# Performance work log

Measured on AMD Instinct MI355X. Metric: run time of the kernel, lower is better.

Reference implementation:

```python
import jax, jax.numpy as jnp
import numpy as np

NPOINT, RADIUS, NSAMPLE = 1024, 0.2, 32
BN_EPS = 1e-5


def _fps(xyz, npoint):
    """Farthest point sampling. xyz: [B,N,3] -> idx [B,npoint]. Deterministic seed (point 0)."""
    B, N, _ = xyz.shape
    init = (jnp.full((B, N), 1e10, xyz.dtype), jnp.zeros((B,), jnp.int32))

    def step(carry, _):
        distance, farthest = carry
        centroid = jnp.take_along_axis(xyz, farthest[:, None, None], axis=1)  # [B,1,3]
        dist = jnp.sum((xyz - centroid) ** 2, -1)                              # [B,N]
        distance = jnp.minimum(distance, dist)
        nxt = jnp.argmax(distance, axis=-1).astype(jnp.int32)
        return (distance, nxt), farthest

    _, cents = jax.lax.scan(step, init, None, length=npoint)  # [npoint,B]
    return cents.T  # [B,npoint]


def _gather(points, idx):
    """points [B,N,C], idx [B,...] -> [B,...,C] (batched fancy indexing)."""
    return jax.vmap(lambda p, i: p[i])(points, idx)


def _square_distance(src, dst):
    # [B,S,3] x [B,N,3] -> [B,S,N]
    d = -2.0 * jnp.einsum('bsc,bnc->bsn', src, dst)
    d += jnp.sum(src ** 2, -1)[:, :, None]
    d += jnp.sum(dst ** 2, -1)[:, None, :]
    return d


def _query_ball(radius, nsample, xyz, new_xyz):
    B, N, _ = xyz.shape
    sqr = _square_distance(new_xyz, xyz)                      # [B,S,N]
    base = jnp.arange(N, dtype=jnp.int32)[None, None, :]
    idx = jnp.where(sqr > radius ** 2, N, base)
    idx = jnp.sort(idx, axis=-1)[:, :, :nsample]              # [B,S,K]
    first = idx[:, :, 0:1]
    idx = jnp.where(idx == N, first, idx)
    return jnp.clip(idx, 0, N - 1)


def _mlp_bn_relu(h, w, b, g, be):
    # h: [B,S,K,Cin]; 1x1 conv == matmul; BN (training-mode batch stats) over (B,S,K).
    y = jnp.einsum('bskc,cd->bskd', h, w) + b
    mu = jnp.mean(y, axis=(0, 1, 2))
    var = jnp.var(y, axis=(0, 1, 2))
    y = (y - mu) * jax.lax.rsqrt(var + BN_EPS) * g + be
    return jax.nn.relu(y)


def setup_inputs():
    key = jax.random.key(0)
    ks = jax.random.split(key, 8)
    B, N, D = 16, 4096, 64
    xyz = jax.random.uniform(ks[0], (B, 3, N), jnp.float32)           # points in unit cube
    points = jax.random.normal(ks[1], (B, D, N), jnp.float32)
    c = [3 + D, 64, 64, 128]
    w0 = jax.random.normal(ks[2], (c[0], c[1]), jnp.float32) * 0.1
    w1 = jax.random.normal(ks[3], (c[1], c[2]), jnp.float32) * 0.1
    w2 = jax.random.normal(ks[4], (c[2], c[3]), jnp.float32) * 0.1
    b0 = jax.random.normal(ks[5], (c[1],), jnp.float32) * 0.05
    b1 = jax.random.normal(ks[6], (c[2],), jnp.float32) * 0.05
    b2 = jax.random.normal(ks[7], (c[3],), jnp.float32) * 0.05
    return dict(xyz=xyz, points=points,
                w0=w0, b0=b0, g0=jnp.ones(c[1]), be0=jnp.zeros(c[1]),
                w1=w1, b1=b1, g1=jnp.ones(c[2]), be1=jnp.zeros(c[2]),
                w2=w2, b2=b2, g2=jnp.ones(c[3]), be2=jnp.zeros(c[3]))


def reference(xyz, points, w0, b0, g0, be0, w1, b1, g1, be1, w2, b2, g2, be2):
    xyz_t = jnp.transpose(xyz, (0, 2, 1))       # [B,N,3]
    pts_t = jnp.transpose(points, (0, 2, 1))    # [B,N,D]
    B, N, _ = xyz_t.shape

    fps_idx = _fps(xyz_t, NPOINT)                               # [B,S]
    new_xyz = _gather(xyz_t, fps_idx)                           # [B,S,3]
    idx = _query_ball(RADIUS, NSAMPLE, xyz_t, new_xyz)          # [B,S,K]
    grouped_xyz = _gather(xyz_t, idx) - new_xyz[:, :, None, :]  # [B,S,K,3]
    grouped_pts = _gather(pts_t, idx)                           # [B,S,K,D]
    h = jnp.concatenate([grouped_xyz, grouped_pts], axis=-1)    # [B,S,K,3+D]

    h = _mlp_bn_relu(h, w0, b0, g0, be0)
    h = _mlp_bn_relu(h, w1, b1, g1, be1)
    h = _mlp_bn_relu(h, w2, b2, g2, be2)
    new_points = jnp.max(h, axis=2)                             # [B,S,Cout]

    return jnp.transpose(new_xyz, (0, 2, 1)), jnp.transpose(new_points, (0, 2, 1))
```

## Files before the change

### kernel.cpp

```cpp
#include <hip/hip_runtime.h>
#include <hip/hip_bf16.h>

typedef unsigned short u16;
typedef short short8 __attribute__((ext_vector_type(8)));
typedef float f32x4 __attribute__((ext_vector_type(4)));

#define NBLK_PASS 4096

#define WS_XYZT   0u
#define WS_PTSH   786432u
#define WS_PTSL   (WS_PTSH + 8388608u)
#define WS_NEWXYZ (WS_PTSL + 8388608u)
#define WS_BALL   (WS_NEWXYZ + 196608u)
#define WS_W0F    (WS_BALL + 2097152u)
#define WS_W1F    (WS_W0F + 24576u)
#define WS_W2F    (WS_W1F + 16384u)
#define WS_P0     (WS_W2F + 32768u)
#define WS_P1     (WS_P0 + 2097152u)
#define WS_P2     (WS_P1 + 2097152u)
#define WS_PR     (WS_P2 + 4194304u)
#define WS_AC0    (WS_PR + 65536u)
#define WS_AC1    (WS_AC0 + 1024u)
#define WS_AC2    (WS_AC1 + 1024u)

__device__ __forceinline__ void split2(float v, u16& h, u16& l) {
  __hip_bfloat16 bh = __float2bfloat16(v);
  float r = v - __bfloat162float(bh);
  __hip_bfloat16 bl = __float2bfloat16(r);
  h = *reinterpret_cast<u16*>(&bh);
  l = *reinterpret_cast<u16*>(&bl);
}

__global__ __launch_bounds__(256) void front_k(
    const float* __restrict__ xyz, const float* __restrict__ pts,
    const float* __restrict__ w0, const float* __restrict__ w1, const float* __restrict__ w2,
    float* __restrict__ xyzT, u16* __restrict__ ptsH, u16* __restrict__ ptsL,
    float* __restrict__ newxyz, float* __restrict__ out0,
    u16* __restrict__ w0f, u16* __restrict__ w1f, u16* __restrict__ w2f)
{
  __shared__ __align__(16) char sm[53312];
  int bid = blockIdx.x, tid = threadIdx.x;

  if (bid < 16) {
    float* lx = (float*)sm; float* ly = lx + 4096; float* lz = ly + 4096;
    int* sIdx = (int*)(sm + 49152);
    unsigned long long* red = (unsigned long long*)(sm + 53248);
    int b = bid, lane = tid & 63, wid = tid >> 6;
    const float4* sx = (const float4*)(xyz + (size_t)(b*3 + 0)*4096);
    const float4* sy = (const float4*)(xyz + (size_t)(b*3 + 1)*4096);
    const float4* sz = (const float4*)(xyz + (size_t)(b*3 + 2)*4096);
    for (int i = tid; i < 1024; i += 256) {
      ((float4*)lx)[i] = sx[i]; ((float4*)ly)[i] = sy[i]; ((float4*)lz)[i] = sz[i];
    }
    __syncthreads();
    float px[16], py[16], pz[16], dist[16];
    #pragma unroll
    for (int i = 0; i < 16; ++i) {
      int p = tid + 256*i;
      px[i] = lx[p]; py[i] = ly[p]; pz[i] = lz[p]; dist[i] = 1e10f;
    }
    unsigned int lo0 = 4095u - (unsigned int)tid;
    int far = 0;
    for (int t = 0; t < 1024; ++t) {
      if (tid == 0) sIdx[t] = far;
      if (t == 1023) break;
      float cx = lx[far], cy = ly[far], cz = lz[far];
      unsigned long long bk = 0ull;
      #pragma unroll
      for (int i = 0; i < 16; ++i) {
        float dx = __fsub_rn(px[i], cx);
        float dy = __fsub_rn(py[i], cy);
        float dz = __fsub_rn(pz[i], cz);
        float d = __fadd_rn(__fadd_rn(__fmul_rn(dx,dx), __fmul_rn(dy,dy)), __fmul_rn(dz,dz));
        float nd = fminf(dist[i], d);
        dist[i] = nd;
        unsigned long long k = ((unsigned long long)__float_as_uint(nd) << 32) | (unsigned long long)(lo0 - 256u*i);
        if (k > bk) bk = k;
      }
      for (int off = 1; off < 64; off <<= 1) {
        unsigned long long o = __shfl_xor(bk, off, 64);
        if (o > bk) bk = o;
      }
      if (lane == 0) red[(t & 1)*4 + wid] = bk;
      __syncthreads();
      unsigned long long m = red[(t & 1)*4 + 0];
      #pragma unroll
      for (int w = 1; w < 4; ++w) { unsigned long long o = red[(t & 1)*4 + w]; if (o > m) m = o; }
      far = 4095 - (int)(unsigned int)(m & 0xffffffffull);
    }
    __syncthreads();
    for (int t = tid; t < 1024; t += 256) {
      int fi = sIdx[t];
      float x = lx[fi], y = ly[fi], z = lz[fi];
      size_t nb = ((size_t)b*1024 + t)*3;
      newxyz[nb + 0] = x; newxyz[nb + 1] = y; newxyz[nb + 2] = z;
      out0[(size_t)(b*3 + 0)*1024 + t] = x;
      out0[(size_t)(b*3 + 1)*1024 + t] = y;
      out0[(size_t)(b*3 + 2)*1024 + t] = z;
    }
  } else if (bid == 16) {
    for (int e = tid; e < 6144; e += 256) {
      int j = e & 7, l = (e >> 3) & 63, ct = (e >> 9) & 3, ks = e >> 11;
      int kk = ks*32 + (l >> 4)*8 + j, col = ct*16 + (l & 15);
      float v = 0.f;
      if (kk < 67) { int orow = (kk < 64) ? (kk + 3) : (kk - 64); v = w0[orow*64 + col]; }
      u16 h, lo; split2(v, h, lo);
      w0f[e] = h; w0f[6144 + e] = lo;
    }
    for (int e = tid; e < 4096; e += 256) {
      int j = e & 7, l = (e >> 3) & 63, ct = (e >> 9) & 3, ks = e >> 11;
      int kk = ks*32 + (l >> 4)*8 + j, col = ct*16 + (l & 15);
      u16 h, lo; split2(w1[kk*64 + col], h, lo);
      w1f[e] = h; w1f[4096 + e] = lo;
    }
    for (int e = tid; e < 8192; e += 256) {
      int j = e & 7, l = (e >> 3) & 63, ct = (e >> 9) & 3, ks = (e >> 11) & 1, cg = e >> 12;
      int kk = ks*32 + (l >> 4)*8 + j, col = cg*64 + ct*16 + (l & 15);
      u16 h, lo; split2(w2[kk*128 + col], h, lo);
      w2f[e] = h; w2f[8192 + e] = lo;
    }
  } else if (bid < 273) {
    int i = (bid - 17)*256 + tid;
    int b = i >> 12, n = i & 4095;
    float x = xyz[(b*3 + 0)*4096 + n];
    float y = xyz[(b*3 + 1)*4096 + n];
    float z = xyz[(b*3 + 2)*4096 + n];
    xyzT[(size_t)i*3 + 0] = x; xyzT[(size_t)i*3 + 1] = y; xyzT[(size_t)i*3 + 2] = z;
  } else {
    int bx = bid - 273;
    u16* th = (u16*)sm;
    u16* tl = th + 64*68;
    int b = bx >> 6, nt = bx & 63;
    int j = tid & 63, dq = tid >> 6;
    #pragma unroll
    for (int db = 0; db < 16; ++db) {
      int d = db*4 + dq;
      float v = pts[((size_t)(b*64 + d))*4096 + nt*64 + j];
      u16 h, lo; split2(v, h, lo);
      th[j*68 + d] = h; tl[j*68 + d] = lo;
    }
    __syncthreads();
    int row = tid >> 2, q = tid & 3;
    size_t o = ((size_t)(b*4096 + nt*64 + row))*64 + q*16;
    const u16* sh = th + row*68 + q*16;
    const u16* sl = tl + row*68 + q*16;
    #pragma unroll
    for (int i = 0; i < 4; ++i) {
      *(uint2*)(ptsH + o + i*4) = *(const uint2*)(sh + i*4);
      *(uint2*)(ptsL + o + i*4) = *(const uint2*)(sl + i*4);
    }
  }
}

__global__ __launch_bounds__(256) void ball_k(const float* __restrict__ xyz,
                                              const float* __restrict__ newxyz,
                                              int* __restrict__ ballidx) {
  __shared__ __align__(16) float lx[4096], ly[4096], lz[4096], ldn[4096];
  int b = blockIdx.x >> 5, tid = threadIdx.x, lane = tid & 63, wid = tid >> 6;
  const float4* sx = (const float4*)(xyz + (size_t)(b*3 + 0)*4096);
  const float4* sy = (const float4*)(xyz + (size_t)(b*3 + 1)*4096);
  const float4* sz = (const float4*)(xyz + (size_t)(b*3 + 2)*4096);
  for (int i = tid; i < 1024; i += 256) {
    ((float4*)lx)[i] = sx[i]; ((float4*)ly)[i] = sy[i]; ((float4*)lz)[i] = sz[i];
  }
  __syncthreads();
  for (int i = tid; i < 4096; i += 256) {
    float x = lx[i], y = ly[i], z = lz[i];
    ldn[i] = __fadd_rn(__fadd_rn(__fmul_rn(x,x), __fmul_rn(y,y)), __fmul_rn(z,z));
  }
  __syncthreads();
  int s0 = (blockIdx.x & 31)*32 + wid*8;
  for (int ci = 0; ci < 8; ++ci) {
    int s = s0 + ci;
    const float* cp = newxyz + ((size_t)b*1024 + s)*3;
    float cx = cp[0], cy = cp[1], cz = cp[2];
    float sn = __fadd_rn(__fadd_rn(__fmul_rn(cx,cx), __fmul_rn(cy,cy)), __fmul_rn(cz,cz));
    int* orow = ballidx + (((size_t)b << 10) + s)*32;
    int cnt = 0, first = -1;
    for (int ch = 0; ch < 64; ++ch) {
      int p = ch*64 + lane;
      float x = lx[p], y = ly[p], z = lz[p];
      float dot = __fmaf_rn(cz, z, __fmaf_rn(cy, y, __fmul_rn(cx, x)));
      float sqr = __fadd_rn(__fadd_rn(__fmul_rn(-2.0f, dot), sn), ldn[p]);
      bool in = !(sqr > 0.04f);
      unsigned long long mask = __ballot(in);
      if (first < 0 && mask) first = ch*64 + (__ffsll((long long)mask) - 1);
      int rank = cnt + __popcll(mask & ((1ull << lane) - 1ull));
      if (in && rank < 32) orow[rank] = p;
      cnt += __popcll(mask);
      if (cnt >= 32) break;
    }
    if (cnt < 32) {
      int fv = (first < 0) ? 4095 : first;
      if (lane >= cnt && lane < 32) orow[lane] = fv;
    }
  }
}

#define LOFF 6144

__device__ __forceinline__ void stats_fin(float* sSt, float* __restrict__ partial,
                                          int C, int tid, int bid) {
  __syncthreads();
  for (int c = tid; c < C; c += 256) {
    float s = sSt[c*2] + sSt[(128 + c)*2] + sSt[(256 + c)*2] + sSt[(384 + c)*2];
    float q = sSt[c*2 + 1] + sSt[(128 + c)*2 + 1] + sSt[(256 + c)*2 + 1] + sSt[(384 + c)*2 + 1];
    partial[(size_t)bid*2*C + c] = s;
    partial[(size_t)bid*2*C + C + c] = q;
  }
}

template<int DEPTH>
__global__ __launch_bounds__(256, 2) void pass_k(
    const int* __restrict__ ballidx,
    const u16* __restrict__ ptsH, const u16* __restrict__ ptsL,
    const float* __restrict__ xyzT, const float* __restrict__ newxyz,
    const u16* __restrict__ w0f, const u16* __restrict__ w1f, const u16* __restrict__ w2f,
    const float* __restrict__ b0, const float* __restrict__ b1, const float* __restrict__ b2,
    const float* __restrict__ ac0, const float* __restrict__ ac1, const float* __restrict__ ac2,
    float* __restrict__ partial, float* __restrict__ outPts)
{
  __shared__ __align__(16) u16 sAh[128*104];
  __shared__ __align__(16) u16 sAl[128*104];
  __shared__ __align__(16) u16 sW[12288];
  int tid = threadIdx.x, lane = tid & 63, wid = tid >> 6;
  int lrow = lane & 15, lkg = lane >> 4;
  int r0 = wid*32;

  {
    int r = tid >> 1, half = tid & 1;
    int R = blockIdx.x*128 + r;
    int b = R >> 15, s = (R & 32767) >> 5;
    int n = ballidx[R];
    size_t o = ((((size_t)b << 12) + n) << 6) + half*32;
    const uint4* srcH = (const uint4*)(ptsH + o);
    const uint4* srcL = (const uint4*)(ptsL + o);
    uint4* dH = (uint4*)(&sAh[r*104 + half*32]);
    uint4* dL = (uint4*)(&sAl[r*104 + half*32]);
    #pragma unroll
    for (int i = 0; i < 4; ++i) { dH[i] = srcH[i]; dL[i] = srcL[i]; }
    if (half) {
      uint4 zz; zz.x = zz.y = zz.z = zz.w = 0u;
      uint4* zH = (uint4*)(&sAh[r*104 + 64]);
      uint4* zL = (uint4*)(&sAl[r*104 + 64]);
      #pragma unroll
      for (int i = 0; i < 4; ++i) { zH[i] = zz; zL[i] = zz; }
      const float* xp = xyzT + (((size_t)b << 12) + n)*3;
      const float* cp = newxyz + (((size_t)b << 10) + s)*3;
      #pragma unroll
      for (int d = 0; d < 3; ++d) {
        u16 h, l; split2(__fsub_rn(xp[d], cp[d]), h, l);
        sAh[r*104 + 64 + d] = h; sAl[r*104 + 64 + d] = l;
      }
    }
  }
  for (int i = tid; i < 768; i += 256) {
    ((uint4*)sW)[i] = ((const uint4*)w0f)[i];
    *(uint4*)(sW + LOFF + i*8) = ((const uint4*)(w0f + 6144))[i];
  }
  __syncthreads();

  f32x4 zv = {0.f, 0.f, 0.f, 0.f};

  f32x4 acc[2][4];
  #pragma unroll
  for (int rt = 0; rt < 2; ++rt)
    #pragma unroll
    for (int ct = 0; ct < 4; ++ct) acc[rt][ct] = zv;
  #pragma unroll
  for (int ks = 0; ks < 3; ++ks) {
    short8 ah[2], al[2];
    #pragma unroll
    for (int rt = 0; rt < 2; ++rt) {
      int ro = (r0 + rt*16 + lrow)*104 + ks*32 + lkg*8;
      ah[rt] = *(const short8*)&sAh[ro];
      al[rt] = *(const short8*)&sAl[ro];
    }
    #pragma unroll
    for (int ct = 0; ct < 4; ++ct) {
      short8 wh = *(const short8*)&sW[((ks*4 + ct)*64 + lane)*8];
      short8 wl = *(const short8*)&sW[LOFF + ((ks*4 + ct)*64 + lane)*8];
      #pragma unroll
      for (int rt = 0; rt < 2; ++rt) {
        acc[rt][ct] = __builtin_amdgcn_mfma_f32_16x16x32_bf16(ah[rt], wh, acc[rt][ct], 0, 0, 0);
        acc[rt][ct] = __builtin_amdgcn_mfma_f32_16x16x32_bf16(al[rt], wh, acc[rt][ct], 0, 0, 0);
        acc[rt][ct] = __builtin_amdgcn_mfma_f32_16x16x32_bf16(ah[rt], wl, acc[rt][ct], 0, 0, 0);
      }
    }
  }

  if constexpr (DEPTH == 1) {
    __syncthreads();
    float* sSt = (float*)sW;
    #pragma unroll
    for (int ct = 0; ct < 4; ++ct) {
      int col = ct*16 + lrow;
      float bv = b0[col], s = 0.f, q = 0.f;
      #pragma unroll
      for (int rt = 0; rt < 2; ++rt)
        #pragma unroll
        for (int r = 0; r < 4; ++r) { float v = acc[rt][ct][r] + bv; s += v; q += v*v; }
      s += __shfl_xor(s, 16, 64); q += __shfl_xor(q, 16, 64);
      s += __shfl_xor(s, 32, 64); q += __shfl_xor(q, 32, 64);
      if (lane < 16) { sSt[(wid*128 + col)*2] = s; sSt[(wid*128 + col)*2 + 1] = q; }
    }
    stats_fin(sSt, partial, 64, tid, blockIdx.x);
    return;
  } else {
    __syncthreads();
    #pragma unroll
    for (int ct = 0; ct < 4; ++ct) {
      int col = ct*16 + lrow;
      float a = ac0[col], cc = fmaf(a, b0[col], ac0[64 + col]);
      #pragma unroll
      for (int rt = 0; rt < 2; ++rt)
        #pragma unroll
        for (int r = 0; r < 4; ++r) {
          float v = fmaxf(fmaf(a, acc[rt][ct][r], cc), 0.f);
          int row = r0 + rt*16 + lkg*4 + r;
          u16 h, l; split2(v, h, l);
          sAh[row*72 + col] = h; sAl[row*72 + col] = l;
        }
    }
    for (int i = tid; i < 512; i += 256) {
      ((uint4*)sW)[i] = ((const uint4*)w1f)[i];
      *(uint4*)(sW + LOFF + i*8) = ((const uint4*)(w1f + 4096))[i];
    }
    __syncthreads();

    #pragma unroll
    for (int rt = 0; rt < 2; ++rt)
      #pragma unroll
      for (int ct = 0; ct < 4; ++ct) acc[rt][ct] = zv;
    #pragma unroll
    for (int ks = 0; ks < 2; ++ks) {
      short8 ah[2], al[2];
      #pragma unroll
      for (int rt = 0; rt < 2; ++rt) {
        int ro = (r0 + rt*16 + lrow)*72 + ks*32 + lkg*8;
        ah[rt] = *(const short8*)&sAh[ro];
        al[rt] = *(const short8*)&sAl[ro];
      }
      #pragma unroll
      for (int ct = 0; ct < 4; ++ct) {
        short8 wh = *(const short8*)&sW[((ks*4 + ct)*64 + lane)*8];
        short8 wl = *(const short8*)&sW[LOFF + ((ks*4 + ct)*64 + lane)*8];
        #pragma unroll
        for (int rt = 0; rt < 2; ++rt) {
          acc[rt][ct] = __builtin_amdgcn_mfma_f32_16x16x32_bf16(ah[rt], wh, acc[rt][ct], 0, 0, 0);
          acc[rt][ct] = __builtin_amdgcn_mfma_f32_16x16x32_bf16(al[rt], wh, acc[rt][ct], 0, 0, 0);
          acc[rt][ct] = __builtin_amdgcn_mfma_f32_16x16x32_bf16(ah[rt], wl, acc[rt][ct], 0, 0, 0);
        }
      }
    }

    if constexpr (DEPTH == 2) {
      __syncthreads();
      float* sSt = (float*)sW;
      #pragma unroll
      for (int ct = 0; ct < 4; ++ct) {
        int col = ct*16 + lrow;
        float bv = b1[col], s = 0.f, q = 0.f;
        #pragma unroll
        for (int rt = 0; rt < 2; ++rt)
          #pragma unroll
          for (int r = 0; r < 4; ++r) { float v = acc[rt][ct][r] + bv; s += v; q += v*v; }
        s += __shfl_xor(s, 16, 64); q += __shfl_xor(q, 16, 64);
        s += __shfl_xor(s, 32, 64); q += __shfl_xor(q, 32, 64);
        if (lane < 16) { sSt[(wid*128 + col)*2] = s; sSt[(wid*128 + col)*2 + 1] = q; }
      }
      stats_fin(sSt, partial, 64, tid, blockIdx.x);
      return;
    } else {
      __syncthreads();
      #pragma unroll
      for (int ct = 0; ct < 4; ++ct) {
        int col = ct*16 + lrow;
        float a = ac1[col], cc = fmaf(a, b1[col], ac1[64 + col]);
        #pragma unroll
        for (int rt = 0; rt < 2; ++rt)
          #pragma unroll
          for (int r = 0; r < 4; ++r) {
            float v = fmaxf(fmaf(a, acc[rt][ct][r], cc), 0.f);
            int row = r0 + rt*16 + lkg*4 + r;
            u16 h, l; split2(v, h, l);
            sAh[row*72 + col] = h; sAl[row*72 + col] = l;
          }
      }
      for (int i = tid; i < 512; i += 256) {
        ((uint4*)sW)[i] = ((const uint4*)w2f)[i];
        *(uint4*)(sW + LOFF + i*8) = ((const uint4*)(w2f + 8192))[i];
      }
      __syncthreads();

      float sc[2][4], sq[2][4];
      #pragma unroll
      for (int cg = 0; cg < 2; ++cg) {
        if (cg) {
          __syncthreads();
          for (int i = tid; i < 512; i += 256) {
            ((uint4*)sW)[i] = ((const uint4*)(w2f + 4096))[i];
            *(uint4*)(sW + LOFF + i*8) = ((const uint4*)(w2f + 12288))[i];
          }
          __syncthreads();
        }
        f32x4 acc2[2][4];
        #pragma unroll
        for (int rt = 0; rt < 2; ++rt)
          #pragma unroll
          for (int ct = 0; ct < 4; ++ct) acc2[rt][ct] = zv;
        #pragma unroll
        for (int ks = 0; ks < 2; ++ks) {
          short8 ah[2], al[2];
          #pragma unroll
          for (int rt = 0; rt < 2; ++rt) {
            int ro = (r0 + rt*16 + lrow)*72 + ks*32 + lkg*8;
            ah[rt] = *(const short8*)&sAh[ro];
            al[rt] = *(const short8*)&sAl[ro];
          }
          #pragma unroll
          for (int ct = 0; ct < 4; ++ct) {
            short8 wh = *(const short8*)&sW[((ks*4 + ct)*64 + lane)*8];
            short8 wl = *(const short8*)&sW[LOFF + ((ks*4 + ct)*64 + lane)*8];
            #pragma unroll
            for (int rt = 0; rt < 2; ++rt) {
              acc2[rt][ct] = __builtin_amdgcn_mfma_f32_16x16x32_bf16(ah[rt], wh, acc2[rt][ct], 0, 0, 0);
              acc2[rt][ct] = __builtin_amdgcn_mfma_f32_16x16x32_bf16(al[rt], wh, acc2[rt][ct], 0, 0, 0);
              acc2[rt][ct] = __builtin_amdgcn_mfma_f32_16x16x32_bf16(ah[rt], wl, acc2[rt][ct], 0, 0, 0);
            }
          }
        }
        if constexpr (DEPTH == 3) {
          #pragma unroll
          for (int ct = 0; ct < 4; ++ct) {
            int col = cg*64 + ct*16 + lrow;
            float bv = b2[col], s = 0.f, q = 0.f;
            #pragma unroll
            for (int rt = 0; rt < 2; ++rt)
              #pragma unroll
              for (int r = 0; r < 4; ++r) { float v = acc2[rt][ct][r] + bv; s += v; q += v*v; }
            s += __shfl_xor(s, 16, 64); q += __shfl_xor(q, 16, 64);
            s += __shfl_xor(s, 32, 64); q += __shfl_xor(q, 32, 64);
            sc[cg][ct] = s; sq[cg][ct] = q;
          }
        } else {
          int G = blockIdx.x*4 + wid;
          int bb = G >> 10, ss = G & 1023;
          #pragma unroll
          for (int ct = 0; ct < 4; ++ct) {
            int col = cg*64 + ct*16 + lrow;
            float a = ac2[col], cc = fmaf(a, b2[col], ac2[128 + col]);
            float m = 0.f;
            #pragma unroll
            for (int rt = 0; rt < 2; ++rt)
              #pragma unroll
              for (int r = 0; r < 4; ++r)
                m = fmaxf(m, fmaxf(fmaf(a, acc2[rt][ct][r], cc), 0.f));
            m = fmaxf(m, __shfl_xor(m, 16, 64));
            m = fmaxf(m, __shfl_xor(m, 32, 64));
            if (lane < 16) outPts[((size_t)bb*128 + col)*1024 + ss] = m;
          }
        }
      }
      if constexpr (DEPTH == 3) {
        __syncthreads();
        float* sSt = (float*)sW;
        if (lane < 16) {
          #pragma unroll
          for (int cg = 0; cg < 2; ++cg)
            #pragma unroll
            for (int ct = 0; ct < 4; ++ct) {
              int col = cg*64 + ct*16 + lrow;
              sSt[(wid*128 + col)*2] = sc[cg][ct];
              sSt[(wid*128 + col)*2 + 1] = sq[cg][ct];
            }
        }
        stats_fin(sSt, partial, 128, tid, blockIdx.x);
      }
    }
  }
}

__global__ void r1_k(const float* __restrict__ partial, int C, float* __restrict__ pr) {
  int j = blockIdx.x, c = threadIdx.x;
  if (c < 2*C) {
    float s = 0.f;
    for (int i = 0; i < 64; ++i) s += partial[((size_t)(j*64 + i))*2*C + c];
    pr[j*2*C + c] = s;
  }
}
__global__ void r2_k(const float* __restrict__ pr, int C,
                     const float* __restrict__ g, const float* __restrict__ be,
                     float* __restrict__ ac) {
  int c = threadIdx.x;
  if (c < C) {
    float s = 0.f, q = 0.f;
    for (int j = 0; j < 64; ++j) { s += pr[j*2*C + c]; q += pr[j*2*C + C + c]; }
    const float inv = 1.0f / 524288.0f;
    float mu = s*inv, var = q*inv - mu*mu;
    float a = g[c] / sqrtf(var + 1e-5f);
    ac[c] = a; ac[C + c] = be[c] - mu*a;
  }
}

extern "C" void kernel_launch(void* const* d_in, const int* in_sizes, int n_in,
                              void* d_out, int out_size, void* d_ws, size_t ws_size,
                              hipStream_t stream) {
  const float* xyz = (const float*)d_in[0];
  const float* pts = (const float*)d_in[1];
  const float* w0  = (const float*)d_in[2];
  const float* b0  = (const float*)d_in[3];
  const float* g0  = (const float*)d_in[4];
  const float* be0 = (const float*)d_in[5];
  const float* w1  = (const float*)d_in[6];
  const float* b1  = (const float*)d_in[7];
  const float* g1  = (const float*)d_in[8];
  const float* be1 = (const float*)d_in[9];
  const float* w2  = (const float*)d_in[10];
  const float* b2  = (const float*)d_in[11];
  const float* g2  = (const float*)d_in[12];
  const float* be2 = (const float*)d_in[13];
  float* out = (float*)d_out;
  char* ws = (char*)d_ws;

  float* xyzT   = (float*)(ws + WS_XYZT);
  u16*   ptsH   = (u16*)(ws + WS_PTSH);
  u16*   ptsL   = (u16*)(ws + WS_PTSL);
  float* newxyz = (float*)(ws + WS_NEWXYZ);
  int*   ballix = (int*)(ws + WS_BALL);
  u16*   w0f    = (u16*)(ws + WS_W0F);
  u16*   w1f    = (u16*)(ws + WS_W1F);
  u16*   w2f    = (u16*)(ws + WS_W2F);
  float* p0     = (float*)(ws + WS_P0);
  float* p1     = (float*)(ws + WS_P1);
  float* p2     = (float*)(ws + WS_P2);
  float* pr     = (float*)(ws + WS_PR);
  float* ac0    = (float*)(ws + WS_AC0);
  float* ac1    = (float*)(ws + WS_AC1);
  float* ac2    = (float*)(ws + WS_AC2);
  float* outPts = out + 49152;

  front_k<<<1297, 256, 0, stream>>>(xyz, pts, w0, w1, w2, xyzT, ptsH, ptsL,
                                    newxyz, out, w0f, w1f, w2f);
  ball_k<<<512, 256, 0, stream>>>(xyz, newxyz, ballix);

  pass_k<1><<<NBLK_PASS, 256, 0, stream>>>(ballix, ptsH, ptsL, xyzT, newxyz,
      w0f, w1f, w2f, b0, b1, b2, ac0, ac1, ac2, p0, outPts);
  r1_k<<<64, 256, 0, stream>>>(p0, 64, pr);
  r2_k<<<1, 256, 0, stream>>>(pr, 64, g0, be0, ac0);

  pass_k<2><<<NBLK_PASS, 256, 0, stream>>>(ballix, ptsH, ptsL, xyzT, newxyz,
      w0f, w1f, w2f, b0, b1, b2, ac0, ac1, ac2, p1, outPts);
  r1_k<<<64, 256, 0, stream>>>(p1, 64, pr);
  r2_k<<<1, 256, 0, stream>>>(pr, 64, g1, be1, ac1);

  pass_k<3><<<NBLK_PASS, 256, 0, stream>>>(ballix, ptsH, ptsL, xyzT, newxyz,
      w0f, w1f, w2f, b0, b1, b2, ac0, ac1, ac2, p2, outPts);
  r1_k<<<64, 256, 0, stream>>>(p2, 128, pr);
  r2_k<<<1, 256, 0, stream>>>(pr, 128, g2, be2, ac2);

  pass_k<4><<<NBLK_PASS, 256, 0, stream>>>(ballix, ptsH, ptsL, xyzT, newxyz,
      w0f, w1f, w2f, b0, b1, b2, ac0, ac1, ac2, p2, outPts);
}
```

Before: 1.115 ms.

## Widen FPS block to 512 threads and use DPP wave reduction for argmax

The farthest-point-sampling front kernel now runs with 512 threads per block, so each thread holds 8 points instead of 16, which shortens the serial per-iteration work. The per-thread argmax now tracks a float and an index rather than packed 64-bit keys. The cross-lane reduction uses DPP row shifts and row broadcasts instead of xor shuffles, and the result is read from lane 63. The block-level reduction grows to 8 wave partials, and the other branches (weight packing, transpose, point split) are retuned for the larger block size. The trade-offs are more per-iteration barrier participants and possible changes in tie-breaking order.

```diff
diff --git a/kernel.cpp b/kernel.cpp
--- a/kernel.cpp
+++ b/kernel.cpp
@@ -31,14 +31,21 @@
   l = *reinterpret_cast<u16*>(&bl);
 }
 
-__global__ __launch_bounds__(256) void front_k(
+#define DPP_MAX64(CTRL) { \
+  unsigned int lo_ = (unsigned int)k, hi_ = (unsigned int)(k >> 32); \
+  unsigned int mlo_ = (unsigned int)__builtin_amdgcn_update_dpp(0, (int)lo_, CTRL, 0xF, 0xF, true); \
+  unsigned int mhi_ = (unsigned int)__builtin_amdgcn_update_dpp(0, (int)hi_, CTRL, 0xF, 0xF, true); \
+  unsigned long long m_ = ((unsigned long long)mhi_ << 32) | mlo_; \
+  if (m_ > k) k = m_; }
+
+__global__ __launch_bounds__(512) void front_k(
     const float* __restrict__ xyz, const float* __restrict__ pts,
     const float* __restrict__ w0, const float* __restrict__ w1, const float* __restrict__ w2,
     float* __restrict__ xyzT, u16* __restrict__ ptsH, u16* __restrict__ ptsL,
     float* __restrict__ newxyz, float* __restrict__ out0,
     u16* __restrict__ w0f, u16* __restrict__ w1f, u16* __restrict__ w2f)
 {
-  __shared__ __align__(16) char sm[53312];
+  __shared__ __align__(16) char sm[53376];
   int bid = blockIdx.x, tid = threadIdx.x;
 
   if (bid < 16) {
@@ -49,14 +56,14 @@
     const float4* sx = (const float4*)(xyz + (size_t)(b*3 + 0)*4096);
     const float4* sy = (const float4*)(xyz + (size_t)(b*3 + 1)*4096);
     const float4* sz = (const float4*)(xyz + (size_t)(b*3 + 2)*4096);
-    for (int i = tid; i < 1024; i += 256) {
+    for (int i = tid; i < 1024; i += 512) {
       ((float4*)lx)[i] = sx[i]; ((float4*)ly)[i] = sy[i]; ((float4*)lz)[i] = sz[i];
     }
     __syncthreads();
-    float px[16], py[16], pz[16], dist[16];
-    #pragma unroll
-    for (int i = 0; i < 16; ++i) {
-      int p = tid + 256*i;
+    float px[8], py[8], pz[8], dist[8];
+    #pragma unroll
+    for (int i = 0; i < 8; ++i) {
+      int p = tid + 512*i;
       px[i] = lx[p]; py[i] = ly[p]; pz[i] = lz[p]; dist[i] = 1e10f;
     }
     unsigned int lo0 = 4095u - (unsigned int)tid;
@@ -65,31 +72,30 @@
       if (tid == 0) sIdx[t] = far;
       if (t == 1023) break;
       float cx = lx[far], cy = ly[far], cz = lz[far];
-      unsigned long long bk = 0ull;
-      #pragma unroll
-      for (int i = 0; i < 16; ++i) {
+      float bestnd = -1.f; unsigned int bestlow = 0u;
+      #pragma unroll
+      for (int i = 0; i < 8; ++i) {
         float dx = __fsub_rn(px[i], cx);
         float dy = __fsub_rn(py[i], cy);
         float dz = __fsub_rn(pz[i], cz);
         float d = __fadd_rn(__fadd_rn(__fmul_rn(dx,dx), __fmul_rn(dy,dy)), __fmul_rn(dz,dz));
         float nd = fminf(dist[i], d);
         dist[i] = nd;
-        unsigned long long k = ((unsigned long long)__float_as_uint(nd) << 32) | (unsigned long long)(lo0 - 256u*i);
-        if (k > bk) bk = k;
-      }
-      for (int off = 1; off < 64; off <<= 1) {
-        unsigned long long o = __shfl_xor(bk, off, 64);
-        if (o > bk) bk = o;
-      }
-      if (lane == 0) red[(t & 1)*4 + wid] = bk;
+        if (nd > bestnd) { bestnd = nd; bestlow = lo0 - 512u*i; }
+      }
+      unsigned long long k = ((unsigned long long)__float_as_uint(bestnd) << 32) | bestlow;
+      DPP_MAX64(0x111) DPP_MAX64(0x112) DPP_MAX64(0x114) DPP_MAX64(0x118)
+      DPP_MAX64(0x142) DPP_MAX64(0x143)
+      if (lane == 63) red[(t & 1)*8 + wid] = k;
       __syncthreads();
-      unsigned long long m = red[(t & 1)*4 + 0];
-      #pragma unroll
-      for (int w = 1; w < 4; ++w) { unsigned long long o = red[(t & 1)*4 + w]; if (o > m) m = o; }
+      const unsigned long long* rr = red + (t & 1)*8;
+      unsigned long long m = rr[0];
+      #pragma unroll
+      for (int w = 1; w < 8; ++w) { unsigned long long o = rr[w]; if (o > m) m = o; }
       far = 4095 - (int)(unsigned int)(m & 0xffffffffull);
     }
     __syncthreads();
-    for (int t = tid; t < 1024; t += 256) {
+    for (int t = tid; t < 1024; t += 512) {
       int fi = sIdx[t];
       float x = lx[fi], y = ly[fi], z = lz[fi];
       size_t nb = ((size_t)b*1024 + t)*3;
@@ -99,7 +105,7 @@
       out0[(size_t)(b*3 + 2)*1024 + t] = z;
     }
   } else if (bid == 16) {
-    for (int e = tid; e < 6144; e += 256) {
+    for (int e = tid; e < 6144; e += 512) {
       int j = e & 7, l = (e >> 3) & 63, ct = (e >> 9) & 3, ks = e >> 11;
       int kk = ks*32 + (l >> 4)*8 + j, col = ct*16 + (l & 15);
       float v = 0.f;
@@ -107,48 +113,47 @@
       u16 h, lo; split2(v, h, lo);
       w0f[e] = h; w0f[6144 + e] = lo;
     }
-    for (int e = tid; e < 4096; e += 256) {
+    for (int e = tid; e < 4096; e += 512) {
       int j = e & 7, l = (e >> 3) & 63, ct = (e >> 9) & 3, ks = e >> 11;
       int kk = ks*32 + (l >> 4)*8 + j, col = ct*16 + (l & 15);
       u16 h, lo; split2(w1[kk*64 + col], h, lo);
       w1f[e] = h; w1f[4096 + e] = lo;
     }
-    for (int e = tid; e < 8192; e += 256) {
+    for (int e = tid; e < 8192; e += 512) {
       int j = e & 7, l = (e >> 3) & 63, ct = (e >> 9) & 3, ks = (e >> 11) & 1, cg = e >> 12;
       int kk = ks*32 + (l >> 4)*8 + j, col = cg*64 + ct*16 + (l & 15);
       u16 h, lo; split2(w2[kk*128 + col], h, lo);
       w2f[e] = h; w2f[8192 + e] = lo;
     }
-  } else if (bid < 273) {
-    int i = (bid - 17)*256 + tid;
+  } else if (bid < 145) {
+    int i = (bid - 17)*512 + tid;
     int b = i >> 12, n = i & 4095;
     float x = xyz[(b*3 + 0)*4096 + n];
     float y = xyz[(b*3 + 1)*4096 + n];
     float z = xyz[(b*3 + 2)*4096 + n];
     xyzT[(size_t)i*3 + 0] = x; xyzT[(size_t)i*3 + 1] = y; xyzT[(size_t)i*3 + 2] = z;
   } else {
-    int bx = bid - 273;
+    int bx = bid - 145;
     u16* th = (u16*)sm;
     u16* tl = th + 64*68;
     int b = bx >> 6, nt = bx & 63;
     int j = tid & 63, dq = tid >> 6;
     #pragma unroll
-    for (int db = 0; db < 16; ++db) {
-      int d = db*4 + dq;
+    for (int db = 0; db < 8; ++db) {
+      int d = db*8 + dq;
       float v = pts[((size_t)(b*64 + d))*4096 + nt*64 + j];
       u16 h, lo; split2(v, h, lo);
       th[j*68 + d] = h; tl[j*68 + d] = lo;
     }
     __syncthreads();
-    int row = tid >> 2, q = tid & 3;
-    size_t o = ((size_t)(b*4096 + nt*64 + row))*64 + q*16;
-    const u16* sh = th + row*68 + q*16;
-    const u16* sl = tl + row*68 + q*16;
-    #pragma unroll
-    for (int i = 0; i < 4; ++i) {
-      *(uint2*)(ptsH + o + i*4) = *(const uint2*)(sh + i*4);
-      *(uint2*)(ptsL + o + i*4) = *(const uint2*)(sl + i*4);
-    }
+    int row = tid >> 3, q = tid & 7;
+    size_t o = ((size_t)(b*4096 + nt*64 + row))*64 + q*8;
+    const u16* sh = th + row*68 + q*8;
+    const u16* sl = tl + row*68 + q*8;
+    uint2 h0 = *(const uint2*)(sh), h1 = *(const uint2*)(sh + 4);
+    uint2 l0 = *(const uint2*)(sl), l1 = *(const uint2*)(sl + 4);
+    *(uint2*)(ptsH + o) = h0; *(uint2*)(ptsH + o + 4) = h1;
+    *(uint2*)(ptsL + o) = l0; *(uint2*)(ptsL + o + 4) = l1;
   }
 }
 
@@ -540,7 +545,7 @@
   float* ac2    = (float*)(ws + WS_AC2);
   float* outPts = out + 49152;
 
-  front_k<<<1297, 256, 0, stream>>>(xyz, pts, w0, w1, w2, xyzT, ptsH, ptsL,
+  front_k<<<1169, 512, 0, stream>>>(xyz, pts, w0, w1, w2, xyzT, ptsH, ptsL,
                                     newxyz, out, w0f, w1f, w2f);
   ball_k<<<512, 256, 0, stream>>>(xyz, newxyz, ballix);
 
```

New measurement: 1.128 ms. Within noise of the previous version (+1.1%).

## Process two FPS batches per block and use DPP wave reductions

Applied to the files above, without the earlier changes.

Farthest point sampling now handles two batch elements per block, interleaving their independent per-step work so the serial chains overlap and share barriers. The 64-bit argmax reduction across a wave uses DPP row shifts and broadcasts instead of shfl_xor, and the per-thread max compares floats before packing the key. This halves the number of FPS blocks and raises per-block shared memory and register use, which may lower occupancy for the other roles in the same kernel.

```diff
diff --git a/kernel.cpp b/kernel.cpp
--- a/kernel.cpp
+++ b/kernel.cpp
@@ -31,74 +31,122 @@
   l = *reinterpret_cast<u16*>(&bl);
 }
 
-__global__ __launch_bounds__(256) void front_k(
+#define DPP_MAX64(K, CTRL) { \
+  unsigned int lo_ = (unsigned int)(K), hi_ = (unsigned int)((K) >> 32); \
+  unsigned int mlo_ = (unsigned int)__builtin_amdgcn_update_dpp(0, (int)lo_, CTRL, 0xF, 0xF, true); \
+  unsigned int mhi_ = (unsigned int)__builtin_amdgcn_update_dpp(0, (int)hi_, CTRL, 0xF, 0xF, true); \
+  unsigned long long m_ = ((unsigned long long)mhi_ << 32) | mlo_; \
+  if (m_ > (K)) (K) = m_; }
+
+#define DPP_CHAIN(K) \
+  DPP_MAX64(K, 0x111) DPP_MAX64(K, 0x112) DPP_MAX64(K, 0x114) DPP_MAX64(K, 0x118) \
+  DPP_MAX64(K, 0x142) DPP_MAX64(K, 0x143)
+
+__global__ __launch_bounds__(256, 1) void front_k(
     const float* __restrict__ xyz, const float* __restrict__ pts,
     const float* __restrict__ w0, const float* __restrict__ w1, const float* __restrict__ w2,
     float* __restrict__ xyzT, u16* __restrict__ ptsH, u16* __restrict__ ptsL,
     float* __restrict__ newxyz, float* __restrict__ out0,
     u16* __restrict__ w0f, u16* __restrict__ w1f, u16* __restrict__ w2f)
 {
-  __shared__ __align__(16) char sm[53312];
+  __shared__ __align__(16) char sm[106752];
   int bid = blockIdx.x, tid = threadIdx.x;
 
-  if (bid < 16) {
-    float* lx = (float*)sm; float* ly = lx + 4096; float* lz = ly + 4096;
-    int* sIdx = (int*)(sm + 49152);
-    unsigned long long* red = (unsigned long long*)(sm + 53248);
-    int b = bid, lane = tid & 63, wid = tid >> 6;
-    const float4* sx = (const float4*)(xyz + (size_t)(b*3 + 0)*4096);
-    const float4* sy = (const float4*)(xyz + (size_t)(b*3 + 1)*4096);
-    const float4* sz = (const float4*)(xyz + (size_t)(b*3 + 2)*4096);
+  if (bid < 8) {
+    float* lxA = (float*)sm;        float* lyA = lxA + 4096; float* lzA = lyA + 4096;
+    float* lxB = lzA + 4096;        float* lyB = lxB + 4096; float* lzB = lyB + 4096;
+    int* sIdxA = (int*)(sm + 98304);
+    int* sIdxB = sIdxA + 1024;
+    unsigned long long* redA = (unsigned long long*)(sm + 106496);
+    unsigned long long* redB = redA + 8;
+    int bA = bid*2, bB = bid*2 + 1;
+    int lane = tid & 63, wid = tid >> 6;
+
+    const float4* sxA = (const float4*)(xyz + (size_t)(bA*3 + 0)*4096);
+    const float4* syA = (const float4*)(xyz + (size_t)(bA*3 + 1)*4096);
+    const float4* szA = (const float4*)(xyz + (size_t)(bA*3 + 2)*4096);
+    const float4* sxB = (const float4*)(xyz + (size_t)(bB*3 + 0)*4096);
+    const float4* syB = (const float4*)(xyz + (size_t)(bB*3 + 1)*4096);
+    const float4* szB = (const float4*)(xyz + (size_t)(bB*3 + 2)*4096);
     for (int i = tid; i < 1024; i += 256) {
-      ((float4*)lx)[i] = sx[i]; ((float4*)ly)[i] = sy[i]; ((float4*)lz)[i] = sz[i];
+      ((float4*)lxA)[i] = sxA[i]; ((float4*)lyA)[i] = syA[i]; ((float4*)lzA)[i] = szA[i];
+      ((float4*)lxB)[i] = sxB[i]; ((float4*)lyB)[i] = syB[i]; ((float4*)lzB)[i] = szB[i];
     }
     __syncthreads();
-    float px[16], py[16], pz[16], dist[16];
+
+    float pxA[16], pyA[16], pzA[16], distA[16];
+    float pxB[16], pyB[16], pzB[16], distB[16];
     #pragma unroll
     for (int i = 0; i < 16; ++i) {
       int p = tid + 256*i;
-      px[i] = lx[p]; py[i] = ly[p]; pz[i] = lz[p]; dist[i] = 1e10f;
+      pxA[i] = lxA[p]; pyA[i] = lyA[p]; pzA[i] = lzA[p]; distA[i] = 1e10f;
+      pxB[i] = lxB[p]; pyB[i] = lyB[p]; pzB[i] = lzB[p]; distB[i] = 1e10f;
     }
     unsigned int lo0 = 4095u - (unsigned int)tid;
-    int far = 0;
+    int farA = 0, farB = 0;
     for (int t = 0; t < 1024; ++t) {
-      if (tid == 0) sIdx[t] = far;
+      if (tid == 0) { sIdxA[t] = farA; sIdxB[t] = farB; }
       if (t == 1023) break;
-      float cx = lx[far], cy = ly[far], cz = lz[far];
-      unsigned long long bk = 0ull;
+      float cxA = lxA[farA], cyA = lyA[farA], czA = lzA[farA];
+      float cxB = lxB[farB], cyB = lyB[farB], czB = lzB[farB];
+
+      float bestndA = -1.f; unsigned int bestlowA = 0u;
       #pragma unroll
       for (int i = 0; i < 16; ++i) {
-        float dx = __fsub_rn(px[i], cx);
-        float dy = __fsub_rn(py[i], cy);
-        float dz = __fsub_rn(pz[i], cz);
+        float dx = __fsub_rn(pxA[i], cxA);
+        float dy = __fsub_rn(pyA[i], cyA);
+        float dz = __fsub_rn(pzA[i], czA);
         float d = __fadd_rn(__fadd_rn(__fmul_rn(dx,dx), __fmul_rn(dy,dy)), __fmul_rn(dz,dz));
-        float nd = fminf(dist[i], d);
-        dist[i] = nd;
-        unsigned long long k = ((unsigned long long)__float_as_uint(nd) << 32) | (unsigned long long)(lo0 - 256u*i);
-        if (k > bk) bk = k;
-      }
-      for (int off = 1; off < 64; off <<= 1) {
-        unsigned long long o = __shfl_xor(bk, off, 64);
-        if (o > bk) bk = o;
-      }
-      if (lane == 0) red[(t & 1)*4 + wid] = bk;
+        float nd = fminf(distA[i], d);
+        distA[i] = nd;
+        if (nd > bestndA) { bestndA = nd; bestlowA = lo0 - 256u*i; }
+      }
+      float bestndB = -1.f; unsigned int bestlowB = 0u;
+      #pragma unroll
+      for (int i = 0; i < 16; ++i) {
+        float dx = __fsub_rn(pxB[i], cxB);
+        float dy = __fsub_rn(pyB[i], cyB);
+        float dz = __fsub_rn(pzB[i], czB);
+        float d = __fadd_rn(__fadd_rn(__fmul_rn(dx,dx), __fmul_rn(dy,dy)), __fmul_rn(dz,dz));
+        float nd = fminf(distB[i], d);
+        distB[i] = nd;
+        if (nd > bestndB) { bestndB = nd; bestlowB = lo0 - 256u*i; }
+      }
+      unsigned long long kA = ((unsigned long long)__float_as_uint(bestndA) << 32) | bestlowA;
+      unsigned long long kB = ((unsigned long long)__float_as_uint(bestndB) << 32) | bestlowB;
+      DPP_CHAIN(kA)
+      DPP_CHAIN(kB)
+      if (lane == 63) { redA[(t & 1)*4 + wid] = kA; redB[(t & 1)*4 + wid] = kB; }
       __syncthreads();
-      unsigned long long m = red[(t & 1)*4 + 0];
-      #pragma unroll
-      for (int w = 1; w < 4; ++w) { unsigned long long o = red[(t & 1)*4 + w]; if (o > m) m = o; }
-      far = 4095 - (int)(unsigned int)(m & 0xffffffffull);
+      const unsigned long long* ra = redA + (t & 1)*4;
+      const unsigned long long* rb = redB + (t & 1)*4;
+      unsigned long long mA = ra[0], mB = rb[0];
+      #pragma unroll
+      for (int w = 1; w < 4; ++w) {
+        unsigned long long oA = ra[w]; if (oA > mA) mA = oA;
+        unsigned long long oB = rb[w]; if (oB > mB) mB = oB;
+      }
+      farA = 4095 - (int)(unsigned int)(mA & 0xffffffffull);
+      farB = 4095 - (int)(unsigned int)(mB & 0xffffffffull);
     }
     __syncthreads();
     for (int t = tid; t < 1024; t += 256) {
-      int fi = sIdx[t];
-      float x = lx[fi], y = ly[fi], z = lz[fi];
-      size_t nb = ((size_t)b*1024 + t)*3;
-      newxyz[nb + 0] = x; newxyz[nb + 1] = y; newxyz[nb + 2] = z;
-      out0[(size_t)(b*3 + 0)*1024 + t] = x;
-      out0[(size_t)(b*3 + 1)*1024 + t] = y;
-      out0[(size_t)(b*3 + 2)*1024 + t] = z;
-    }
-  } else if (bid == 16) {
+      int fiA = sIdxA[t];
+      float xA = lxA[fiA], yA = lyA[fiA], zA = lzA[fiA];
+      size_t nbA = ((size_t)bA*1024 + t)*3;
+      newxyz[nbA + 0] = xA; newxyz[nbA + 1] = yA; newxyz[nbA + 2] = zA;
+      out0[(size_t)(bA*3 + 0)*1024 + t] = xA;
+      out0[(size_t)(bA*3 + 1)*1024 + t] = yA;
+      out0[(size_t)(bA*3 + 2)*1024 + t] = zA;
+      int fiB = sIdxB[t];
+      float xB = lxB[fiB], yB = lyB[fiB], zB = lzB[fiB];
+      size_t nbB = ((size_t)bB*1024 + t)*3;
+      newxyz[nbB + 0] = xB; newxyz[nbB + 1] = yB; newxyz[nbB + 2] = zB;
+      out0[(size_t)(bB*3 + 0)*1024 + t] = xB;
+      out0[(size_t)(bB*3 + 1)*1024 + t] = yB;
+      out0[(size_t)(bB*3 + 2)*1024 + t] = zB;
+    }
+  } else if (bid == 8) {
     for (int e = tid; e < 6144; e += 256) {
       int j = e & 7, l = (e >> 3) & 63, ct = (e >> 9) & 3, ks = e >> 11;
       int kk = ks*32 + (l >> 4)*8 + j, col = ct*16 + (l & 15);
@@ -119,15 +167,15 @@
       u16 h, lo; split2(w2[kk*128 + col], h, lo);
       w2f[e] = h; w2f[8192 + e] = lo;
     }
-  } else if (bid < 273) {
-    int i = (bid - 17)*256 + tid;
+  } else if (bid < 265) {
+    int i = (bid - 9)*256 + tid;
     int b = i >> 12, n = i & 4095;
     float x = xyz[(b*3 + 0)*4096 + n];
     float y = xyz[(b*3 + 1)*4096 + n];
     float z = xyz[(b*3 + 2)*4096 + n];
     xyzT[(size_t)i*3 + 0] = x; xyzT[(size_t)i*3 + 1] = y; xyzT[(size_t)i*3 + 2] = z;
   } else {
-    int bx = bid - 273;
+    int bx = bid - 265;
     u16* th = (u16*)sm;
     u16* tl = th + 64*68;
     int b = bx >> 6, nt = bx & 63;
@@ -540,7 +588,7 @@
   float* ac2    = (float*)(ws + WS_AC2);
   float* outPts = out + 49152;
 
-  front_k<<<1297, 256, 0, stream>>>(xyz, pts, w0, w1, w2, xyzT, ptsH, ptsL,
+  front_k<<<1289, 256, 0, stream>>>(xyz, pts, w0, w1, w2, xyzT, ptsH, ptsL,
                                     newxyz, out, w0f, w1f, w2f);
   ball_k<<<512, 256, 0, stream>>>(xyz, newxyz, ballix);
 
```

New measurement: 1.400 ms. +25.6%, slower.
